# Kernel optimization log

Measured on AMD Instinct MI355X. Metric: run time of the kernel, lower is better.

Reference implementation:

```python
import jax, jax.numpy as jnp
import numpy as np

N_COUNTIES = 3144
P = 2
N_MOB = 6
N_COV = 10
T = 156
NNZ = 31440


def setup_inputs() -> dict:
    key = jax.random.key(0)
    ks = jax.random.split(key, 13)
    C = jax.random.uniform(ks[0], (T, N_COUNTIES), dtype=jnp.float32)
    D = jax.random.uniform(ks[1], (T, N_COUNTIES), dtype=jnp.float32)
    M = jax.random.uniform(ks[2], (N_MOB, T, N_COUNTIES), dtype=jnp.float32)
    cov = jax.random.normal(ks[3], (N_COV, N_COUNTIES), dtype=jnp.float32)
    B_nonzero = jax.random.normal(ks[4], (NNZ,), dtype=jnp.float32)
    A_nonzero = jax.random.normal(ks[5], (NNZ,), dtype=jnp.float32)
    H_nonzero = jax.random.normal(ks[6], (NNZ,), dtype=jnp.float32)
    mu = jax.random.normal(ks[7], (N_MOB, P), dtype=jnp.float32)
    nu = jax.random.normal(ks[8], (N_MOB, P), dtype=jnp.float32)
    upsilon = jax.random.normal(ks[9], (N_COV,), dtype=jnp.float32)
    zeta = jax.random.normal(ks[10], (N_COV,), dtype=jnp.float32)
    rows = jax.random.randint(ks[11], (NNZ,), 0, N_COUNTIES)
    cols = jax.random.randint(ks[12], (NNZ,), 0, N_COUNTIES)
    return dict(C=C, D=D, M=M, cov=cov, B_nonzero=B_nonzero, A_nonzero=A_nonzero,
                H_nonzero=H_nonzero, mu=mu, nu=nu, upsilon=upsilon, zeta=zeta,
                rows=rows, cols=cols)


def reference(C, D, M, cov, B_nonzero, A_nonzero, H_nonzero, mu, nu, upsilon, zeta, rows, cols):
    n = C.shape[1]
    p = mu.shape[1]
    Tp = C.shape[0] - p  # number of predicted steps (t = p .. T-1)

    # Dense scatter-built weight matrices (duplicates summed, matching
    # torch.sparse .to_dense()). The torch code reuses the SAME nonzero
    # vector for every lag tau, so B[tau] == B for all tau.
    B = jnp.zeros((n, n), C.dtype).at[rows, cols].add(B_nonzero)
    A = jnp.zeros((n, n), C.dtype).at[rows, cols].add(A_nonzero)
    H = jnp.zeros((n, n), C.dtype).at[rows, cols].add(H_nonzero)

    # Lagged windows: Cl[tau, i] = C[i + tau] == C[t - p + tau] for t = p + i.
    Cl = jnp.stack([C[tau:tau + Tp] for tau in range(p)], 0)  # [p, Tp, n]
    Dl = jnp.stack([D[tau:tau + Tp] for tau in range(p)], 0)  # [p, Tp, n]
    Ml = jnp.stack([M[:, tau:tau + Tp, :] for tau in range(p)], 1)  # [n_mob, p, Tp, n]

    # Since B[tau] are identical across lags, sum over p folds into one GEMM.
    c2c = jnp.einsum('ptn,nm->tm', Cl, B)  # [Tp, n]
    c2d = jnp.einsum('ptn,nm->tm', Cl, H)
    d2d = jnp.einsum('ptn,nm->tm', Dl, A)

    mob_c = jnp.einsum('kptn,kp->tn', Ml, mu)
    mob_d = jnp.einsum('kptn,kp->tn', Ml, nu)

    C_hat = c2c + mob_c + upsilon @ cov  # [Tp, n] (+ broadcast [n])
    D_hat = c2d + d2d + mob_d + zeta @ cov
    return C_hat, D_hat
```

## Files before the change

kernel.cpp:

```cpp
#include <hip/hip_runtime.h>


#define BS      256
#define ECAP    64
#define SPILLC  4096
#define SCAN_TH 1024
#define POISON  0xAAAAAAAAu

__global__ void prep(const int* __restrict__ rows, const int* __restrict__ cols,
                     const float* __restrict__ Bnz, const float* __restrict__ Anz,
                     const float* __restrict__ Hnz,
                     const float* __restrict__ C, const float* __restrict__ D,
                     float2* __restrict__ CsDs,
                     float4* __restrict__ edges, unsigned* __restrict__ cnt,
                     unsigned* __restrict__ spill_cnt, int* __restrict__ spill,
                     int T, int NC, int NNZ, int TPn, int fillBlocks, int tT64) {
    if ((int)blockIdx.x < fillBlocks) {
        int k = blockIdx.x * BS + threadIdx.x;
        if (k < NNZ) {
            int c = cols[k];
            unsigned j = atomicAdd(&cnt[c], 1u) - POISON;
            if (j < ECAP)
                edges[(size_t)c * ECAP + j] =
                    make_float4(__int_as_float(rows[k]), Bnz[k], Anz[k], Hnz[k]);
            else {
                unsigned sp = atomicAdd(spill_cnt, 1u) - POISON;
                if (sp < SPILLC) spill[sp] = k;
            }
        }
        return;
    }
    __shared__ float tc[65][65], td[65][65];
    int bid = blockIdx.x - fillBlocks;
    int ct = bid / tT64, tt = bid - ct * tT64;
    int lx = threadIdx.x & 63, ly = threadIdx.x >> 6;
    int c0 = ct * 64, t0 = tt * 64;
    for (int rr = ly; rr < 65; rr += 4) {
        int t = t0 + rr, c = c0 + lx;
        if (t < T && c < NC) {
            tc[rr][lx] = C[(size_t)t * NC + c];
            td[rr][lx] = D[(size_t)t * NC + c];
        }
    }
    __syncthreads();
    for (int rr = ly; rr < 64; rr += 4) {
        int c = c0 + rr, t = t0 + lx;
        if (c < NC && t < TPn)
            CsDs[(size_t)c * TPn + t] =
                make_float2(tc[lx][rr] + tc[lx + 1][rr],
                            td[lx][rr] + td[lx + 1][rr]);
    }
}

__global__ void sparse_wave(const float2* __restrict__ CsDs,
                            const unsigned* __restrict__ cnt, const float4* __restrict__ edges,
                            float2* __restrict__ wsS,
                            int TPn, int nChunks, int nWaves) {
    int gtid = blockIdx.x * blockDim.x + threadIdx.x;
    int wid = gtid >> 6, lane = threadIdx.x & 63;
    if (wid >= nWaves) return;
    int c = wid / nChunks;
    int chunk = wid - c * nChunks;
    int cu = __builtin_amdgcn_readfirstlane(c);
    int i = chunk * 64 + lane;
    bool valid = i < TPn;
    int isafe = valid ? i : (TPn - 1);
    float a0 = 0.f, a1 = 0.f;
    unsigned n = cnt[cu] - POISON;
    if (n > ECAP) n = ECAP;
    const float4* eb = edges + (size_t)cu * ECAP;
    for (unsigned j = 0; j < n; ++j) {
        float4 E = eb[j];
        int g = __float_as_int(E.x);
        float2 v = CsDs[(size_t)g * TPn + isafe];
        a0 += v.x * E.y;
        a1 += v.x * E.w + v.y * E.z;
    }
    if (valid) wsS[(size_t)c * TPn + i] = make_float2(a0, a1);
}

#define FTI 32
#define FTC 32
__global__ void final_fuse(const float2* __restrict__ wsS,
                           const float* __restrict__ M,
                           const float* __restrict__ cov,
                           const float* __restrict__ mu,
                           const float* __restrict__ nu,
                           const float* __restrict__ ups, const float* __restrict__ zet,
                           const float2* __restrict__ CsDs,
                           const int* __restrict__ rows, const int* __restrict__ cols,
                           const float* __restrict__ Bnz, const float* __restrict__ Anz,
                           const float* __restrict__ Hnz,
                           const unsigned* __restrict__ spill_cnt, const int* __restrict__ spill,
                           float* __restrict__ out0, float* __restrict__ out1,
                           int T, int NC, int TPn, int cTiles) {
    __shared__ float s0[FTI][FTC + 1], s1[FTI][FTC + 1];
    int bi = blockIdx.x / cTiles;
    int bc = blockIdx.x - bi * cTiles;
    int i0 = bi * FTI, c0 = bc * FTC;
    int tid = threadIdx.x;

    {
        int li = tid & 31;
        int lc0 = tid >> 5;
        int i = i0 + li;
        for (int cc = lc0; cc < FTC; cc += 8) {
            int c = c0 + cc;
            float2 v = make_float2(0.f, 0.f);
            if (c < NC && i < TPn) v = wsS[(size_t)c * TPn + i];
            s0[li][cc] = v.x;
            s1[li][cc] = v.y;
        }
    }
    __syncthreads();

    int lc = tid & 31;
    int ri = tid >> 5;
    int c = c0 + lc;
    if (c < NC) {
        float cv0 = 0.f, cv1 = 0.f;
#pragma unroll
        for (int j = 0; j < 10; ++j) {
            float cv = cov[(size_t)j * NC + c];
            cv0 += cv * ups[j];
            cv1 += cv * zet[j];
        }
        int iiBeg = ri * 4;
        int iFirst = i0 + iiBeg;
        if (iFirst < TPn) {
            float m0r[6];
#pragma unroll
            for (int k = 0; k < 6; ++k)
                m0r[k] = M[((size_t)k * T + iFirst) * NC + c];
#pragma unroll
            for (int ii = 0; ii < 4; ++ii) {
                int i = iFirst + ii;
                if (i >= TPn) break;
                float a0 = s0[iiBeg + ii][lc] + cv0;
                float a1 = s1[iiBeg + ii][lc] + cv1;
#pragma unroll
                for (int k = 0; k < 6; ++k) {
                    float m1 = M[((size_t)k * T + i + 1) * NC + c];
                    a0 += m0r[k] * mu[k * 2] + m1 * mu[k * 2 + 1];
                    a1 += m0r[k] * nu[k * 2] + m1 * nu[k * 2 + 1];
                    m0r[k] = m1;
                }
                out0[(size_t)i * NC + c] = a0;
                out1[(size_t)i * NC + c] = a1;
            }
        }
    }

    unsigned nsp = *spill_cnt - POISON;
    if (nsp != 0) {
        __syncthreads();
        if (nsp > SPILLC) nsp = SPILLC;
        int cmax = NC - c0; if (cmax > FTC) cmax = FTC;
        if (tid < FTI) {
            int io = i0 + tid;
            if (io < TPn) {
                for (unsigned s = 0; s < nsp; ++s) {
                    int k = spill[s];
                    int cc = cols[k];
                    if (cc >= c0 && cc < c0 + cmax) {
                        int g = rows[k];
                        float2 v = CsDs[(size_t)g * TPn + io];
                        atomicAdd(&out0[(size_t)io * NC + cc], v.x * Bnz[k]);
                        atomicAdd(&out1[(size_t)io * NC + cc], v.x * Hnz[k] + v.y * Anz[k]);
                    }
                }
            }
        }
    }
}

__global__ void csr_hist(const int* __restrict__ cols, int* __restrict__ counts, int NNZ) {
    int k = blockIdx.x * blockDim.x + threadIdx.x;
    if (k < NNZ) atomicAdd(&counts[cols[k]], 1);
}
__global__ __launch_bounds__(SCAN_TH)
void csr_scan(const int* __restrict__ counts, int* __restrict__ offsets,
              int* __restrict__ cursor, int NC) {
    __shared__ int ssum[SCAN_TH];
    int t = threadIdx.x;
    int chunk = (NC + SCAN_TH - 1) / SCAN_TH;
    int beg = t * chunk, end = min(beg + chunk, NC);
    int local = 0;
    for (int j = beg; j < end; ++j) local += counts[j];
    ssum[t] = local;
    __syncthreads();
    for (int off = 1; off < SCAN_TH; off <<= 1) {
        int v = (t >= off) ? ssum[t - off] : 0;
        __syncthreads();
        ssum[t] += v;
        __syncthreads();
    }
    int run = ssum[t] - local;
    for (int j = beg; j < end; ++j) {
        offsets[j] = run;
        cursor[j]  = run;
        run += counts[j];
    }
    if (t == SCAN_TH - 1) offsets[NC] = ssum[SCAN_TH - 1];
}
__global__ void csr_fill(const int* __restrict__ rows, const int* __restrict__ cols,
                         const float* __restrict__ Bnz, const float* __restrict__ Anz,
                         const float* __restrict__ Hnz,
                         int* __restrict__ cursor, float4* __restrict__ edges, int NNZ) {
    int k = blockIdx.x * blockDim.x + threadIdx.x;
    if (k >= NNZ) return;
    int s = cols[k];
    int pos = atomicAdd(&cursor[s], 1);
    edges[pos] = make_float4(__int_as_float(rows[k]), Bnz[k], Anz[k], Hnz[k]);
}
__global__ void fused_generic(const float* __restrict__ C, const float* __restrict__ D,
                              const float* __restrict__ M, const float* __restrict__ cov,
                              const float* __restrict__ mu, const float* __restrict__ nu,
                              const float* __restrict__ ups, const float* __restrict__ zet,
                              const int* __restrict__ offsets, const float4* __restrict__ edges,
                              float* __restrict__ out0, float* __restrict__ out1,
                              int T, int NC, int NMOB, int NCOV, int P, int TPn) {
    int idx = blockIdx.x * blockDim.x + threadIdx.x;
    if (idx >= TPn * NC) return;
    int i = idx / NC;
    int c = idx - i * NC;
    float acc0 = 0.f, acc1 = 0.f;
    for (int k = 0; k < NMOB; ++k)
        for (int tau = 0; tau < P; ++tau) {
            float m = M[((size_t)k * T + i + tau) * NC + c];
            acc0 += m * mu[k * P + tau];
            acc1 += m * nu[k * P + tau];
        }
    for (int j = 0; j < NCOV; ++j) {
        float cv = cov[(size_t)j * NC + c];
        acc0 += cv * ups[j];
        acc1 += cv * zet[j];
    }
    int e0 = offsets[c], e1 = offsets[c + 1];
    for (int e = e0; e < e1; ++e) {
        float4 E = edges[e];
        int g = __float_as_int(E.x);
        float cs = 0.f, ds = 0.f;
        for (int tau = 0; tau < P; ++tau) {
            cs += C[(size_t)(i + tau) * NC + g];
            ds += D[(size_t)(i + tau) * NC + g];
        }
        acc0 += cs * E.y;
        acc1 += cs * E.w + ds * E.z;
    }
    out0[idx] = acc0;
    out1[idx] = acc1;
}

extern "C" void kernel_launch(void* const* d_in, const int* in_sizes, int n_in,
                              void* d_out, int out_size, void* d_ws, size_t ws_size,
                              hipStream_t stream) {
    const float* C    = (const float*)d_in[0];
    const float* D    = (const float*)d_in[1];
    const float* M    = (const float*)d_in[2];
    const float* cov  = (const float*)d_in[3];
    const float* Bnz  = (const float*)d_in[4];
    const float* Anz  = (const float*)d_in[5];
    const float* Hnz  = (const float*)d_in[6];
    const float* mu   = (const float*)d_in[7];
    const float* nu   = (const float*)d_in[8];
    const float* ups  = (const float*)d_in[9];
    const float* zet  = (const float*)d_in[10];
    const int*  rows  = (const int*)d_in[11];
    const int*  cols  = (const int*)d_in[12];

    int NCOV = in_sizes[9];
    int NC   = in_sizes[3] / NCOV;
    int T    = in_sizes[0] / NC;
    int NMOB = in_sizes[2] / in_sizes[0];
    int P    = in_sizes[7] / NMOB;
    int NNZ  = in_sizes[11];
    int TPn  = T - P;

    float* out0 = (float*)d_out;
    float* out1 = out0 + (size_t)TPn * NC;

    float4*   edges  = (float4*)d_ws;
    unsigned* cnt    = (unsigned*)(edges + (size_t)NC * ECAP);
    unsigned* spillc = cnt + NC;
    int*      spill  = (int*)(spillc + 1);
    uintptr_t pa     = (uintptr_t)(spill + SPILLC);
    pa               = (pa + 15) & ~(uintptr_t)15;
    float2*   CsDs   = (float2*)pa;
    float2*   wsS    = CsDs + (size_t)NC * TPn;
    size_t    need   = (size_t)((char*)(wsS + (size_t)NC * TPn) - (char*)d_ws);

    if (P == 2 && NMOB == 6 && NCOV == 10 && ws_size >= need) {
        int fillBlocks = (NNZ + BS - 1) / BS;
        int cT64 = (NC + 63) / 64, tT64 = (T + 63) / 64;
        prep<<<fillBlocks + cT64 * tT64, BS, 0, stream>>>(
            rows, cols, Bnz, Anz, Hnz, C, D, CsDs,
            edges, cnt, spillc, spill, T, NC, NNZ, TPn, fillBlocks, tT64);

        int nChunks = (TPn + 63) / 64;
        int nWaves  = NC * nChunks;
        sparse_wave<<<(nWaves * 64 + BS - 1) / BS, BS, 0, stream>>>(
            CsDs, cnt, edges, wsS, TPn, nChunks, nWaves);

        int iTiles = (TPn + FTI - 1) / FTI;
        int cTiles = (NC + FTC - 1) / FTC;
        final_fuse<<<iTiles * cTiles, BS, 0, stream>>>(
            wsS, M, cov, mu, nu, ups, zet, CsDs,
            rows, cols, Bnz, Anz, Hnz, spillc, spill,
            out0, out1, T, NC, TPn, cTiles);
    } else {
        float4* fedges   = (float4*)d_ws;
        int*    foffsets = (int*)(fedges + NNZ);
        int*    fcounts  = foffsets + (NC + 1);
        int*    fcursor  = fcounts + NC;
        hipMemsetAsync(fcounts, 0, (size_t)NC * sizeof(int), stream);
        csr_hist<<<(NNZ + BS - 1) / BS, BS, 0, stream>>>(cols, fcounts, NNZ);
        csr_scan<<<1, SCAN_TH, 0, stream>>>(fcounts, foffsets, fcursor, NC);
        csr_fill<<<(NNZ + BS - 1) / BS, BS, 0, stream>>>(
            rows, cols, Bnz, Anz, Hnz, fcursor, fedges, NNZ);
        int n = TPn * NC;
        fused_generic<<<(n + BS - 1) / BS, BS, 0, stream>>>(
            C, D, M, cov, mu, nu, ups, zet, foffsets, fedges,
            out0, out1, T, NC, NMOB, NCOV, P, TPn);
    }
}
```

Measured before the change: 115.6 us.

## Fuse sparse gather and epilogue into one kernel over column-parallel threads

Replaces the sparse_wave and final_fuse kernels with one kernel. Each thread owns one column and two consecutive time steps, does the per-column edge gather with float4 loads of CsDs, and adds the mobility, covariate and spill terms before writing the outputs directly. This drops the wsS intermediate round-trip and one launch. In exchange, the CsDs gather is now strided across lanes (each lane reads a different column's edge list and a different source row) rather than contiguous in time, lanes with different edge counts diverge, and the spill loop is scanned per thread. The fast path also now requires an even TPn.

Result: slower. 127.5 us (+10.3%).

```diff
diff --git a/kernel.cpp b/kernel.cpp
--- a/kernel.cpp
+++ b/kernel.cpp
@@ -52,126 +52,81 @@
     }
 }
 
-__global__ void sparse_wave(const float2* __restrict__ CsDs,
-                            const unsigned* __restrict__ cnt, const float4* __restrict__ edges,
-                            float2* __restrict__ wsS,
-                            int TPn, int nChunks, int nWaves) {
-    int gtid = blockIdx.x * blockDim.x + threadIdx.x;
-    int wid = gtid >> 6, lane = threadIdx.x & 63;
-    if (wid >= nWaves) return;
-    int c = wid / nChunks;
-    int chunk = wid - c * nChunks;
-    int cu = __builtin_amdgcn_readfirstlane(c);
-    int i = chunk * 64 + lane;
-    bool valid = i < TPn;
-    int isafe = valid ? i : (TPn - 1);
-    float a0 = 0.f, a1 = 0.f;
-    unsigned n = cnt[cu] - POISON;
+__global__ void mega(const float2* __restrict__ CsDs,
+                     const unsigned* __restrict__ cnt, const float4* __restrict__ edges,
+                     const float* __restrict__ M,
+                     const float* __restrict__ cov,
+                     const float* __restrict__ mu,
+                     const float* __restrict__ nu,
+                     const float* __restrict__ ups, const float* __restrict__ zet,
+                     const int* __restrict__ rows, const int* __restrict__ cols,
+                     const float* __restrict__ Bnz, const float* __restrict__ Anz,
+                     const float* __restrict__ Hnz,
+                     const unsigned* __restrict__ spill_cnt, const int* __restrict__ spill,
+                     float* __restrict__ out0, float* __restrict__ out1,
+                     int T, int NC, int TPn) {
+    int c = blockIdx.x * blockDim.x + threadIdx.x;
+    if (c >= NC) return;
+    int i0 = (int)blockIdx.y * 2;
+
+    unsigned n = cnt[c] - POISON;
     if (n > ECAP) n = ECAP;
-    const float4* eb = edges + (size_t)cu * ECAP;
+    const float4* eb = edges + (size_t)c * ECAP;
+    float s00 = 0.f, s01 = 0.f, s10 = 0.f, s11 = 0.f;
     for (unsigned j = 0; j < n; ++j) {
         float4 E = eb[j];
         int g = __float_as_int(E.x);
-        float2 v = CsDs[(size_t)g * TPn + isafe];
-        a0 += v.x * E.y;
-        a1 += v.x * E.w + v.y * E.z;
-    }
-    if (valid) wsS[(size_t)c * TPn + i] = make_float2(a0, a1);
-}
-
-#define FTI 32
-#define FTC 32
-__global__ void final_fuse(const float2* __restrict__ wsS,
-                           const float* __restrict__ M,
-                           const float* __restrict__ cov,
-                           const float* __restrict__ mu,
-                           const float* __restrict__ nu,
-                           const float* __restrict__ ups, const float* __restrict__ zet,
-                           const float2* __restrict__ CsDs,
-                           const int* __restrict__ rows, const int* __restrict__ cols,
-                           const float* __restrict__ Bnz, const float* __restrict__ Anz,
-                           const float* __restrict__ Hnz,
-                           const unsigned* __restrict__ spill_cnt, const int* __restrict__ spill,
-                           float* __restrict__ out0, float* __restrict__ out1,
-                           int T, int NC, int TPn, int cTiles) {
-    __shared__ float s0[FTI][FTC + 1], s1[FTI][FTC + 1];
-    int bi = blockIdx.x / cTiles;
-    int bc = blockIdx.x - bi * cTiles;
-    int i0 = bi * FTI, c0 = bc * FTC;
-    int tid = threadIdx.x;
-
-    {
-        int li = tid & 31;
-        int lc0 = tid >> 5;
-        int i = i0 + li;
-        for (int cc = lc0; cc < FTC; cc += 8) {
-            int c = c0 + cc;
-            float2 v = make_float2(0.f, 0.f);
-            if (c < NC && i < TPn) v = wsS[(size_t)c * TPn + i];
-            s0[li][cc] = v.x;
-            s1[li][cc] = v.y;
-        }
-    }
-    __syncthreads();
-
-    int lc = tid & 31;
-    int ri = tid >> 5;
-    int c = c0 + lc;
-    if (c < NC) {
-        float cv0 = 0.f, cv1 = 0.f;
+        float4 v = *(const float4*)(CsDs + (size_t)g * TPn + i0);
+        s00 += v.x * E.y;
+        s01 += v.x * E.w + v.y * E.z;
+        s10 += v.z * E.y;
+        s11 += v.z * E.w + v.w * E.z;
+    }
+
+    float cv0 = 0.f, cv1 = 0.f;
 #pragma unroll
-        for (int j = 0; j < 10; ++j) {
-            float cv = cov[(size_t)j * NC + c];
-            cv0 += cv * ups[j];
-            cv1 += cv * zet[j];
-        }
-        int iiBeg = ri * 4;
-        int iFirst = i0 + iiBeg;
-        if (iFirst < TPn) {
-            float m0r[6];
+    for (int j = 0; j < 10; ++j) {
+        float cv = cov[(size_t)j * NC + c];
+        cv0 += cv * ups[j];
+        cv1 += cv * zet[j];
+    }
+    float a00 = s00 + cv0, a01 = s01 + cv1;
+    float a10 = s10 + cv0, a11 = s11 + cv1;
+
 #pragma unroll
-            for (int k = 0; k < 6; ++k)
-                m0r[k] = M[((size_t)k * T + iFirst) * NC + c];
-#pragma unroll
-            for (int ii = 0; ii < 4; ++ii) {
-                int i = iFirst + ii;
-                if (i >= TPn) break;
-                float a0 = s0[iiBeg + ii][lc] + cv0;
-                float a1 = s1[iiBeg + ii][lc] + cv1;
-#pragma unroll
-                for (int k = 0; k < 6; ++k) {
-                    float m1 = M[((size_t)k * T + i + 1) * NC + c];
-                    a0 += m0r[k] * mu[k * 2] + m1 * mu[k * 2 + 1];
-                    a1 += m0r[k] * nu[k * 2] + m1 * nu[k * 2 + 1];
-                    m0r[k] = m1;
-                }
-                out0[(size_t)i * NC + c] = a0;
-                out1[(size_t)i * NC + c] = a1;
-            }
-        }
+    for (int k = 0; k < 6; ++k) {
+        const float* Mk = M + (size_t)(k * T + i0) * NC + c;
+        float m0 = Mk[0];
+        float m1 = Mk[(size_t)NC];
+        float m2 = Mk[(size_t)2 * NC];
+        float u0 = mu[k * 2], u1 = mu[k * 2 + 1];
+        float w0 = nu[k * 2], w1 = nu[k * 2 + 1];
+        a00 += m0 * u0 + m1 * u1;
+        a01 += m0 * w0 + m1 * w1;
+        a10 += m1 * u0 + m2 * u1;
+        a11 += m1 * w0 + m2 * w1;
     }
 
     unsigned nsp = *spill_cnt - POISON;
     if (nsp != 0) {
-        __syncthreads();
         if (nsp > SPILLC) nsp = SPILLC;
-        int cmax = NC - c0; if (cmax > FTC) cmax = FTC;
-        if (tid < FTI) {
-            int io = i0 + tid;
-            if (io < TPn) {
-                for (unsigned s = 0; s < nsp; ++s) {
-                    int k = spill[s];
-                    int cc = cols[k];
-                    if (cc >= c0 && cc < c0 + cmax) {
-                        int g = rows[k];
-                        float2 v = CsDs[(size_t)g * TPn + io];
-                        atomicAdd(&out0[(size_t)io * NC + cc], v.x * Bnz[k]);
-                        atomicAdd(&out1[(size_t)io * NC + cc], v.x * Hnz[k] + v.y * Anz[k]);
-                    }
-                }
+        for (unsigned s = 0; s < nsp; ++s) {
+            int k = spill[s];
+            if (cols[k] == c) {
+                int g = rows[k];
+                float4 v = *(const float4*)(CsDs + (size_t)g * TPn + i0);
+                a00 += v.x * Bnz[k];
+                a01 += v.x * Hnz[k] + v.y * Anz[k];
+                a10 += v.z * Bnz[k];
+                a11 += v.z * Hnz[k] + v.w * Anz[k];
             }
         }
     }
+
+    out0[(size_t)i0 * NC + c] = a00;
+    out1[(size_t)i0 * NC + c] = a01;
+    out0[(size_t)(i0 + 1) * NC + c] = a10;
+    out1[(size_t)(i0 + 1) * NC + c] = a11;
 }
 
 __global__ void csr_hist(const int* __restrict__ cols, int* __restrict__ counts, int NNZ) {
@@ -287,27 +242,21 @@
     uintptr_t pa     = (uintptr_t)(spill + SPILLC);
     pa               = (pa + 15) & ~(uintptr_t)15;
     float2*   CsDs   = (float2*)pa;
-    float2*   wsS    = CsDs + (size_t)NC * TPn;
-    size_t    need   = (size_t)((char*)(wsS + (size_t)NC * TPn) - (char*)d_ws);
-
-    if (P == 2 && NMOB == 6 && NCOV == 10 && ws_size >= need) {
+    size_t    need   = (size_t)((char*)(CsDs + (size_t)NC * TPn) - (char*)d_ws);
+
+    if (P == 2 && NMOB == 6 && NCOV == 10 && TPn > 0 && (TPn & 1) == 0 &&
+        ws_size >= need) {
         int fillBlocks = (NNZ + BS - 1) / BS;
         int cT64 = (NC + 63) / 64, tT64 = (T + 63) / 64;
         prep<<<fillBlocks + cT64 * tT64, BS, 0, stream>>>(
             rows, cols, Bnz, Anz, Hnz, C, D, CsDs,
             edges, cnt, spillc, spill, T, NC, NNZ, TPn, fillBlocks, tT64);
 
-        int nChunks = (TPn + 63) / 64;
-        int nWaves  = NC * nChunks;
-        sparse_wave<<<(nWaves * 64 + BS - 1) / BS, BS, 0, stream>>>(
-            CsDs, cnt, edges, wsS, TPn, nChunks, nWaves);
-
-        int iTiles = (TPn + FTI - 1) / FTI;
-        int cTiles = (NC + FTC - 1) / FTC;
-        final_fuse<<<iTiles * cTiles, BS, 0, stream>>>(
-            wsS, M, cov, mu, nu, ups, zet, CsDs,
+        dim3 mg((NC + BS - 1) / BS, TPn / 2);
+        mega<<<mg, BS, 0, stream>>>(
+            CsDs, cnt, edges, M, cov, mu, nu, ups, zet,
             rows, cols, Bnz, Anz, Hnz, spillc, spill,
-            out0, out1, T, NC, TPn, cTiles);
+            out0, out1, T, NC, TPn);
     } else {
         float4* fedges   = (float4*)d_ws;
         int*    foffsets = (int*)(fedges + NNZ);
```
